# Kernel tuning notes

Hardware: AMD Instinct MI355X
Metric: run time of the kernel (lower is better)

## Reference

```python
import jax, jax.numpy as jnp
import numpy as np

N_NODES = 50000
N_EDGES = 800000
D = 64  # node_dim == edge_dim
NEG_SLOPE = 0.2
EPS = 1e-5


def _lin_params(key, d_in, d_out):
    k1, k2 = jax.random.split(key)
    bound = 1.0 / np.sqrt(d_in)
    W = jax.random.uniform(k1, (d_out, d_in), minval=-bound, maxval=bound, dtype=jnp.float32)
    b = jax.random.uniform(k2, (d_out,), minval=-bound, maxval=bound, dtype=jnp.float32)
    return W, b


def setup_inputs() -> dict:
    key = jax.random.key(0)
    ks = jax.random.split(key, 12)
    V = jax.random.normal(ks[0], (N_NODES, D), dtype=jnp.float32)
    E = jax.random.normal(ks[1], (N_EDGES, D), dtype=jnp.float32)
    src = jax.random.randint(ks[2], (N_EDGES,), 0, N_NODES, dtype=jnp.int32)
    dst = jax.random.randint(ks[3], (N_EDGES,), 0, N_NODES, dtype=jnp.int32)
    pA_w, pA_b = _lin_params(ks[4], D, D)   # NodePooling.A
    pB_w, pB_b = _lin_params(ks[5], D, D)   # NodePooling.B
    mW1, mb1 = _lin_params(ks[6], D, D)     # edge MLP layer 1
    mW2, mb2 = _lin_params(ks[7], D, D)     # edge MLP layer 2
    BW, Bb = _lin_params(ks[8], D, D)       # GenMessage.B (scale)
    CW, Cb = _lin_params(ks[9], D, D)       # GenMessage.C (shift)
    return {"V": V, "E": E, "src": src, "dst": dst,
            "pA_w": pA_w, "pA_b": pA_b, "pB_w": pB_w, "pB_b": pB_b,
            "mW1": mW1, "mb1": mb1, "mW2": mW2, "mb2": mb2,
            "BW": BW, "Bb": Bb, "CW": CW, "Cb": Cb}


def _lrelu(x):
    return jnp.where(x >= 0, x, NEG_SLOPE * x)


def reference(V, E, src, dst, pA_w, pA_b, pB_w, pB_b, mW1, mb1, mW2, mb2, BW, Bb, CW, Cb):
    n = V.shape[0]
    # V = act(V); NodePooling: B(lrelu(A(V)))
    Va = _lrelu(V)
    Vp = _lrelu(Va @ pA_w.T + pA_b) @ pB_w.T + pB_b  # [N, D]
    # edge MLP on edge features (2 Linear+ReLU layers)
    x = jax.nn.relu(E @ mW1.T + mb1)
    x = jax.nn.relu(x @ mW2.T + mb2)                  # [E, D]
    scale = jax.nn.sigmoid(x @ BW.T + Bb)
    shift = x @ CW.T + Cb
    # gathered src features, gated affine message
    M1 = scale * Vp[src] + shift                      # [E, D]
    M2 = M1 * M1
    # segment-mean onto dst (DGL fn.mean); zero for isolated nodes
    deg = jax.ops.segment_sum(jnp.ones((dst.shape[0],), jnp.float32), dst, num_segments=n)
    denom = jnp.maximum(deg, 1.0)[:, None]
    V1 = jax.ops.segment_sum(M1, dst, num_segments=n) / denom
    V2 = jax.ops.segment_sum(M2, dst, num_segments=n) / denom
    return jnp.sqrt(jax.nn.relu(V2 - V1) + EPS)
```

## Files before the change

### kernel.cpp

```cpp
#include <hip/hip_runtime.h>

#define NN 50000
#define NE 800000
#define DDIM 64
#define PADX 68
#define PADS 68
#define NB_SCAN ((NN + 255) / 256)
#define NEG_SLOPE 0.2f
#define EPS_V 1e-5f

typedef short bf16x8 __attribute__((ext_vector_type(8)));
typedef float f32x4 __attribute__((ext_vector_type(4)));

__device__ __forceinline__ float lrelu_f(float x) { return x >= 0.0f ? x : NEG_SLOPE * x; }

__device__ __forceinline__ unsigned short bf16_rn(float x) {
    union { float f; unsigned int u; } c; c.f = x;
    unsigned int r = c.u + 0x7FFF + ((c.u >> 16) & 1);
    return (unsigned short)(r >> 16);
}
__device__ __forceinline__ float bf16_tof(unsigned short h) {
    union { float f; unsigned int u; } c; c.u = ((unsigned int)h) << 16;
    return c.f;
}

__device__ __forceinline__ void split8(const float* __restrict__ v, bf16x8& h, bf16x8& l)
{
    #pragma unroll
    for (int j = 0; j < 8; ++j) {
        unsigned short hh = bf16_rn(v[j]);
        h[j] = (short)hh;
        l[j] = (short)bf16_rn(v[j] - bf16_tof(hh));
    }
}

__device__ __forceinline__ void mma_tile(float acc[16], const float* __restrict__ XT,
                                         const float* __restrict__ Wc, int e0, int f0)
{
    #pragma unroll 4
    for (int kk = 0; kk < DDIM; kk += 4) {
        float4 A0 = *(const float4*)&XT[(kk+0)*PADX + e0];
        float4 A1 = *(const float4*)&XT[(kk+1)*PADX + e0];
        float4 A2 = *(const float4*)&XT[(kk+2)*PADX + e0];
        float4 A3 = *(const float4*)&XT[(kk+3)*PADX + e0];
        float4 B0 = *(const float4*)&Wc[(f0+0)*PADX + kk];
        float4 B1 = *(const float4*)&Wc[(f0+1)*PADX + kk];
        float4 B2 = *(const float4*)&Wc[(f0+2)*PADX + kk];
        float4 B3 = *(const float4*)&Wc[(f0+3)*PADX + kk];
        const float a[4][4] = {{A0.x,A0.y,A0.z,A0.w},{A1.x,A1.y,A1.z,A1.w},
                               {A2.x,A2.y,A2.z,A2.w},{A3.x,A3.y,A3.z,A3.w}};
        const float b[4][4] = {{B0.x,B0.y,B0.z,B0.w},{B1.x,B1.y,B1.z,B1.w},
                               {B2.x,B2.y,B2.z,B2.w},{B3.x,B3.y,B3.z,B3.w}};
        #pragma unroll
        for (int j = 0; j < 4; ++j)
            #pragma unroll
            for (int i = 0; i < 4; ++i)
                #pragma unroll
                for (int q = 0; q < 4; ++q)
                    acc[i*4+j] = fmaf(a[q][i], b[j][q], acc[i*4+j]);
    }
}

__device__ __forceinline__ void load_w_f32(float* __restrict__ Wc, const float* __restrict__ Wg, int tid)
{
    #pragma unroll
    for (int c = 0; c < 4; ++c) {
        int idx = (c << 10) + (tid << 2);
        int f = idx >> 6, k = idx & 63;
        *(float4*)&Wc[f*PADX + k] = *(const float4*)&Wg[idx];
    }
}

__global__ __launch_bounds__(256, 3)
void node_pool_kernel(const float* __restrict__ V,
                      const float* __restrict__ Aw, const float* __restrict__ Ab,
                      const float* __restrict__ Bw, const float* __restrict__ Bbv,
                      float* __restrict__ Vp,
                      const int* __restrict__ dst, int* __restrict__ degi)
{
    __shared__ float Wc[DDIM*PADX];
    __shared__ float XT[DDIM*PADX];
    const int tid = threadIdx.x;
    const int nb = blockIdx.x * 64;
    const int e0 = (tid & 15) << 2;
    const int f0 = (tid >> 4) << 2;

    #pragma unroll
    for (int c = 0; c < 4; ++c) {
        int idx = (c << 10) + (tid << 2);
        int e = idx >> 6, d = idx & 63;
        int row = nb + e; if (row > NN-1) row = NN-1;
        float4 v = *(const float4*)&V[(size_t)row*DDIM + d];
        XT[(d+0)*PADX + e] = lrelu_f(v.x);
        XT[(d+1)*PADX + e] = lrelu_f(v.y);
        XT[(d+2)*PADX + e] = lrelu_f(v.z);
        XT[(d+3)*PADX + e] = lrelu_f(v.w);
    }
    load_w_f32(Wc, Aw, tid);
    __syncthreads();

    float acc[16];
    #pragma unroll
    for (int i = 0; i < 16; ++i) acc[i] = 0.f;
    mma_tile(acc, XT, Wc, e0, f0);
    __syncthreads();

    {
        float4 bv = *(const float4*)&Ab[f0];
        const float ba[4] = {bv.x, bv.y, bv.z, bv.w};
        #pragma unroll
        for (int j = 0; j < 4; ++j) {
            float4 v;
            v.x = lrelu_f(acc[0*4+j] + ba[j]);
            v.y = lrelu_f(acc[1*4+j] + ba[j]);
            v.z = lrelu_f(acc[2*4+j] + ba[j]);
            v.w = lrelu_f(acc[3*4+j] + ba[j]);
            *(float4*)&XT[(f0+j)*PADX + e0] = v;
        }
    }
    load_w_f32(Wc, Bw, tid);
    __syncthreads();

    float acc2[16];
    #pragma unroll
    for (int i = 0; i < 16; ++i) acc2[i] = 0.f;
    mma_tile(acc2, XT, Wc, e0, f0);

    float4 bv = *(const float4*)&Bbv[f0];
    #pragma unroll
    for (int i = 0; i < 4; ++i) {
        int row = nb + e0 + i;
        if (row < NN) {
            float4 o;
            o.x = acc2[i*4+0] + bv.x;
            o.y = acc2[i*4+1] + bv.y;
            o.z = acc2[i*4+2] + bv.z;
            o.w = acc2[i*4+3] + bv.w;
            *(float4*)&Vp[(size_t)row*DDIM + f0] = o;
        }
    }

    const int stride = gridDim.x * 256;
    for (int e = blockIdx.x * 256 + tid; e < NE; e += stride)
        atomicAdd(&degi[dst[e]], 1);
}

__global__ __launch_bounds__(256)
void prep_w_kernel(const float* __restrict__ W1, const float* __restrict__ W2,
                   const float* __restrict__ WB, const float* __restrict__ WC,
                   short* __restrict__ WF)
{
    int gid = blockIdx.x * 256 + threadIdx.x;
    int L = gid >> 12, r = gid & 4095;
    int t = r >> 10, ks = (r >> 9) & 1, lane = (r >> 3) & 63, j = r & 7;
    const float* Ws = (L == 0) ? W1 : (L == 1) ? W2 : (L == 2) ? WB : WC;
    int n = lane & 15, kg = lane >> 4;
    int f = t*16 + n, k = ks*32 + kg*8 + j;
    float v = Ws[f*64 + k];
    unsigned short h = bf16_rn(v);
    unsigned short l = bf16_rn(v - bf16_tof(h));
    int base = L*8192 + ((t*2 + ks)*2)*512 + lane*8 + j;
    WF[base]       = (short)h;
    WF[base + 512] = (short)l;
}

__global__ __launch_bounds__(256)
void scan1_kernel(const int* __restrict__ degi, int* __restrict__ linc, int* __restrict__ bsum)
{
    __shared__ int ws[4];
    const int tid = threadIdx.x;
    const int lane = tid & 63, wv = tid >> 6;
    int i = blockIdx.x * 256 + tid;
    int v = (i < NN) ? degi[i] : 0;
    int sc = v;
    #pragma unroll
    for (int off = 1; off < 64; off <<= 1) {
        int t = __shfl_up(sc, off, 64);
        if (lane >= off) sc += t;
    }
    if (lane == 63) ws[wv] = sc;
    __syncthreads();
    int wb = 0;
    #pragma unroll
    for (int w = 0; w < 4; ++w) if (w < wv) wb += ws[w];
    int incl = sc + wb;
    if (i < NN) linc[i] = incl;
    if (tid == 255) bsum[blockIdx.x] = incl;
}

__global__ __launch_bounds__(256)
void scan23_kernel(const int* __restrict__ degi, const int* __restrict__ linc,
                   const int* __restrict__ bsum, int* __restrict__ curs)
{
    __shared__ int ws[4];
    __shared__ int base_s;
    const int tid = threadIdx.x;
    const int lane = tid & 63, wv = tid >> 6;
    int v = (tid < NB_SCAN) ? bsum[tid] : 0;
    int sc = v;
    #pragma unroll
    for (int off = 1; off < 64; off <<= 1) {
        int t = __shfl_up(sc, off, 64);
        if (lane >= off) sc += t;
    }
    if (lane == 63) ws[wv] = sc;
    __syncthreads();
    int wb = 0;
    #pragma unroll
    for (int w = 0; w < 4; ++w) if (w < wv) wb += ws[w];
    if (tid == blockIdx.x) base_s = sc + wb - v;
    __syncthreads();
    int i = blockIdx.x * 256 + tid;
    if (i < NN) curs[i] = base_s + linc[i] - degi[i];
}

__global__ __launch_bounds__(256)
void scatter_kernel(const int* __restrict__ dst, int* __restrict__ cursor, int* __restrict__ eidx)
{
    int e = blockIdx.x * 256 + threadIdx.x;
    if (e < NE) {
        int p = atomicAdd(&cursor[dst[e]], 1);
        eidx[p] = e;
    }
}

__device__ __forceinline__ void gemm64_dual(const short* __restrict__ WL, int lane,
                                            const bf16x8 ah0[2], const bf16x8 al0[2],
                                            const bf16x8 ah1[2], const bf16x8 al1[2],
                                            f32x4 acc0[4], f32x4 acc1[4])
{
    #pragma unroll
    for (int ks = 0; ks < 2; ++ks) {
        bf16x8 bh[4], bl[4];
        #pragma unroll
        for (int t = 0; t < 4; ++t) {
            bh[t] = *(const bf16x8*)&WL[(((t*2 + ks)*2 + 0)*64 + lane)*8];
            bl[t] = *(const bf16x8*)&WL[(((t*2 + ks)*2 + 1)*64 + lane)*8];
        }
        #pragma unroll
        for (int t = 0; t < 4; ++t) {
            acc0[t] = __builtin_amdgcn_mfma_f32_16x16x32_bf16(al0[ks], bh[t], acc0[t], 0, 0, 0);
            acc1[t] = __builtin_amdgcn_mfma_f32_16x16x32_bf16(al1[ks], bh[t], acc1[t], 0, 0, 0);
            acc0[t] = __builtin_amdgcn_mfma_f32_16x16x32_bf16(ah0[ks], bl[t], acc0[t], 0, 0, 0);
            acc1[t] = __builtin_amdgcn_mfma_f32_16x16x32_bf16(ah1[ks], bl[t], acc1[t], 0, 0, 0);
            acc0[t] = __builtin_amdgcn_mfma_f32_16x16x32_bf16(ah0[ks], bh[t], acc0[t], 0, 0, 0);
            acc1[t] = __builtin_amdgcn_mfma_f32_16x16x32_bf16(ah1[ks], bh[t], acc1[t], 0, 0, 0);
        }
    }
}

__device__ __forceinline__ void transpose_frags_dual(float* __restrict__ sw,
                                                     const f32x4 y0[4], const f32x4 y1[4],
                                                     int lane,
                                                     bf16x8 ah0[2], bf16x8 al0[2],
                                                     bf16x8 ah1[2], bf16x8 al1[2])
{
    const int n = lane & 15, mg = lane >> 4;
    #pragma unroll
    for (int t = 0; t < 4; ++t)
        #pragma unroll
        for (int r = 0; r < 4; ++r) {
            sw[(mg*4 + r)*PADS + t*16 + n]      = y0[t][r];
            sw[(16 + mg*4 + r)*PADS + t*16 + n] = y1[t][r];
        }
    __builtin_amdgcn_wave_barrier();
    const int m = lane & 15, kg = lane >> 4;
    {
        float x[16];
        *(float4*)&x[0]  = *(const float4*)&sw[m*PADS + kg*8];
        *(float4*)&x[4]  = *(const float4*)&sw[m*PADS + kg*8 + 4];
        *(float4*)&x[8]  = *(const float4*)&sw[m*PADS + 32 + kg*8];
        *(float4*)&x[12] = *(const float4*)&sw[m*PADS + 32 + kg*8 + 4];
        split8(&x[0], ah0[0], al0[0]);
        split8(&x[8], ah0[1], al0[1]);
    }
    {
        float x[16];
        *(float4*)&x[0]  = *(const float4*)&sw[(16+m)*PADS + kg*8];
        *(float4*)&x[4]  = *(const float4*)&sw[(16+m)*PADS + kg*8 + 4];
        *(float4*)&x[8]  = *(const float4*)&sw[(16+m)*PADS + 32 + kg*8];
        *(float4*)&x[12] = *(const float4*)&sw[(16+m)*PADS + 32 + kg*8 + 4];
        split8(&x[0], ah1[0], al1[0]);
        split8(&x[8], ah1[1], al1[1]);
    }
    __builtin_amdgcn_wave_barrier();
}

__global__ __launch_bounds__(256, 3)
void edge_kernel(const float* __restrict__ Eg,
                 const int* __restrict__ src, const int* __restrict__ dst,
                 const int* __restrict__ eidx,
                 const short* __restrict__ WF,
                 const float* __restrict__ b1, const float* __restrict__ b2,
                 const float* __restrict__ bB, const float* __restrict__ bC,
                 const float* __restrict__ Vp,
                 float* __restrict__ S1, float* __restrict__ S2)
{
    __shared__ float scratch[4 * 32 * PADS];
    __shared__ int aux[4 * 64];

    const int tid = threadIdx.x;
    const int lane = tid & 63, wv = tid >> 6;
    float* sw = scratch + wv * 32 * PADS;
    int* auxw = aux + wv * 64;

    const int ew = blockIdx.x * 128 + wv * 32;
    const int m = lane & 15, kg = lane >> 4;

    if (lane < 32) {
        int eg = eidx[ew + lane];
        auxw[lane]      = src[eg];
        auxw[32 + lane] = dst[eg];
    }
    bf16x8 ah0[2], al0[2], ah1[2], al1[2];
    {
        int eg0 = eidx[ew + m];
        int eg1 = eidx[ew + 16 + m];
        const float* er0 = Eg + (size_t)eg0*DDIM + kg*8;
        const float* er1 = Eg + (size_t)eg1*DDIM + kg*8;
        float x[16];
        *(float4*)&x[0]  = *(const float4*)&er0[0];
        *(float4*)&x[4]  = *(const float4*)&er0[4];
        *(float4*)&x[8]  = *(const float4*)&er0[32];
        *(float4*)&x[12] = *(const float4*)&er0[36];
        split8(&x[0], ah0[0], al0[0]);
        split8(&x[8], ah0[1], al0[1]);
        *(float4*)&x[0]  = *(const float4*)&er1[0];
        *(float4*)&x[4]  = *(const float4*)&er1[4];
        *(float4*)&x[8]  = *(const float4*)&er1[32];
        *(float4*)&x[12] = *(const float4*)&er1[36];
        split8(&x[0], ah1[0], al1[0]);
        split8(&x[8], ah1[1], al1[1]);
    }

    const int n = lane & 15, mg = lane >> 4;

    f32x4 acc0[4], acc1[4];
    #pragma unroll
    for (int t = 0; t < 4; ++t) { acc0[t] = (f32x4){0.f,0.f,0.f,0.f}; acc1[t] = (f32x4){0.f,0.f,0.f,0.f}; }
    gemm64_dual(WF, lane, ah0, al0, ah1, al1, acc0, acc1);
    #pragma unroll
    for (int t = 0; t < 4; ++t) {
        float b = b1[t*16 + n];
        #pragma unroll
        for (int r = 0; r < 4; ++r) {
            acc0[t][r] = fmaxf(acc0[t][r] + b, 0.0f);
            acc1[t][r] = fmaxf(acc1[t][r] + b, 0.0f);
        }
    }
    transpose_frags_dual(sw, acc0, acc1, lane, ah0, al0, ah1, al1);

    #pragma unroll
    for (int t = 0; t < 4; ++t) { acc0[t] = (f32x4){0.f,0.f,0.f,0.f}; acc1[t] = (f32x4){0.f,0.f,0.f,0.f}; }
    gemm64_dual(WF + 8192, lane, ah0, al0, ah1, al1, acc0, acc1);
    #pragma unroll
    for (int t = 0; t < 4; ++t) {
        float b = b2[t*16 + n];
        #pragma unroll
        for (int r = 0; r < 4; ++r) {
            acc0[t][r] = fmaxf(acc0[t][r] + b, 0.0f);
            acc1[t][r] = fmaxf(acc1[t][r] + b, 0.0f);
        }
    }
    transpose_frags_dual(sw, acc0, acc1, lane, ah0, al0, ah1, al1);

    f32x4 accS0[4], accS1[4], accH0[4], accH1[4];
    #pragma unroll
    for (int t = 0; t < 4; ++t) {
        accS0[t] = (f32x4){0.f,0.f,0.f,0.f}; accS1[t] = (f32x4){0.f,0.f,0.f,0.f};
        accH0[t] = (f32x4){0.f,0.f,0.f,0.f}; accH1[t] = (f32x4){0.f,0.f,0.f,0.f};
    }
    gemm64_dual(WF + 2*8192, lane, ah0, al0, ah1, al1, accS0, accS1);
    gemm64_dual(WF + 3*8192, lane, ah0, al0, ah1, al1, accH0, accH1);

    {
        int sn0[4], sn1[4];
        #pragma unroll
        for (int r = 0; r < 4; ++r) { sn0[r] = auxw[mg*4 + r]; sn1[r] = auxw[16 + mg*4 + r]; }
        #pragma unroll
        for (int t = 0; t < 4; ++t) {
            const int f = t*16 + n;
            const float bBv = bB[f];
            const float bCv = bC[f];
            #pragma unroll
            for (int r = 0; r < 4; ++r) {
                float vp0 = Vp[(size_t)sn0[r]*DDIM + f];
                float sg0 = 1.0f / (1.0f + __expf(-(accS0[t][r] + bBv)));
                sw[(mg*4 + r)*PADS + f] = fmaf(sg0, vp0, accH0[t][r] + bCv);
                float vp1 = Vp[(size_t)sn1[r]*DDIM + f];
                float sg1 = 1.0f / (1.0f + __expf(-(accS1[t][r] + bBv)));
                sw[(16 + mg*4 + r)*PADS + f] = fmaf(sg1, vp1, accH1[t][r] + bCv);
            }
        }
    }
    __builtin_amdgcn_wave_barrier();

    const int f = lane;
    float s1 = 0.f, s2 = 0.f;
    int prev = auxw[32];
    #pragma unroll 4
    for (int e = 0; e < 32; ++e) {
        int dn = auxw[32 + e];
        float m1 = sw[e*PADS + f];
        float m2 = m1 * m1;
        if (dn != prev) {
            atomicAdd(&S1[(size_t)prev*DDIM + f], s1);
            atomicAdd(&S2[(size_t)prev*DDIM + f], s2);
            s1 = 0.f; s2 = 0.f; prev = dn;
        }
        s1 += m1; s2 += m2;
    }
    atomicAdd(&S1[(size_t)prev*DDIM + f], s1);
    atomicAdd(&S2[(size_t)prev*DDIM + f], s2);
}

__global__ __launch_bounds__(256)
void finalize_kernel(const float* __restrict__ S1, const float* __restrict__ S2,
                     const int* __restrict__ degi, float* __restrict__ out)
{
    int gid = blockIdx.x * blockDim.x + threadIdx.x;
    if (gid >= NN*DDIM) return;
    int n = gid >> 6;
    float dn = (float)degi[n];
    dn = dn > 1.0f ? dn : 1.0f;
    float v = (S2[gid] - S1[gid]) / dn;
    out[gid] = sqrtf(fmaxf(v, 0.0f) + EPS_V);
}

extern "C" void kernel_launch(void* const* d_in, const int* in_sizes, int n_in,
                              void* d_out, int out_size, void* d_ws, size_t ws_size,
                              hipStream_t stream) {
    const float* V   = (const float*)d_in[0];
    const float* Eg  = (const float*)d_in[1];
    const int*   src = (const int*)d_in[2];
    const int*   dst = (const int*)d_in[3];
    const float* pAw = (const float*)d_in[4];
    const float* pAb = (const float*)d_in[5];
    const float* pBw = (const float*)d_in[6];
    const float* pBb = (const float*)d_in[7];
    const float* mW1 = (const float*)d_in[8];
    const float* mb1 = (const float*)d_in[9];
    const float* mW2 = (const float*)d_in[10];
    const float* mb2 = (const float*)d_in[11];
    const float* BW  = (const float*)d_in[12];
    const float* Bb  = (const float*)d_in[13];
    const float* CW  = (const float*)d_in[14];
    const float* Cb  = (const float*)d_in[15];
    float* out = (float*)d_out;

    float* ws    = (float*)d_ws;
    float* Vp    = ws;
    float* S1    = ws + (size_t)NN*DDIM;
    float* S2    = ws + (size_t)2*NN*DDIM;
    int*   degi  = (int*)(ws + (size_t)3*NN*DDIM);
    int*   curs  = degi + NN;
    int*   linc  = curs + NN;
    int*   bsum  = linc + NN;
    int*   bbase = bsum + NB_SCAN;
    int*   eidx  = bbase + NB_SCAN;
    short* WF    = (short*)(eidx + NE);

    hipMemsetAsync(S1, 0, (size_t)(2*NN*DDIM + NN) * sizeof(float), stream);

    prep_w_kernel<<<64, 256, 0, stream>>>(mW1, mW2, BW, CW, WF);
    node_pool_kernel<<<(NN + 63)/64, 256, 0, stream>>>(V, pAw, pAb, pBw, pBb, Vp, dst, degi);
    scan1_kernel<<<NB_SCAN, 256, 0, stream>>>(degi, linc, bsum);
    scan23_kernel<<<NB_SCAN, 256, 0, stream>>>(degi, linc, bsum, curs);
    scatter_kernel<<<(NE + 255)/256, 256, 0, stream>>>(dst, curs, eidx);
    edge_kernel<<<NE/128, 256, 0, stream>>>(Eg, src, dst, eidx, WF,
                                            mb1, mb2, Bb, Cb, Vp, S1, S2);
    finalize_kernel<<<(NN*DDIM + 255)/256, 256, 0, stream>>>(S1, S2, degi, out);
}
```

Measured before the change: 577.7 us.

## Make edge kernel persistent over contiguous sorted groups with plain stores for interior segments

The edge kernel now launches a fixed 4096 waves, and each wave walks a contiguous range of 32-edge groups in dst-sorted order. Running segment sums carry across groups, so a node segment that lies wholly inside one wave's range is written with plain stores. Only the first and last segments of each range still use atomics. The bf16 hi/lo split also switches to the packed v_cvt_pk_bf16_f32 instruction. The trade-off is less parallelism and latency hiding per launch, since each wave now runs its groups serially.

Result: slower. 788.1 us (+36.4%).

```diff
diff --git a/kernel.cpp b/kernel.cpp
--- a/kernel.cpp
+++ b/kernel.cpp
@@ -9,6 +9,11 @@
 #define NEG_SLOPE 0.2f
 #define EPS_V 1e-5f
 
+#define NGROUPS (NE / 32)
+#define NWAVES_E 4096
+#define GQ (NGROUPS / NWAVES_E)
+#define GR (NGROUPS - NWAVES_E * GQ)
+
 typedef short bf16x8 __attribute__((ext_vector_type(8)));
 typedef float f32x4 __attribute__((ext_vector_type(4)));
 
@@ -24,14 +29,27 @@
     return c.f;
 }
 
+__device__ __forceinline__ unsigned cvtpk_bf16(float a, float b) {
+    unsigned r;
+    asm("v_cvt_pk_bf16_f32 %0, %1, %2" : "=v"(r) : "v"(a), "v"(b));
+    return r;
+}
+
 __device__ __forceinline__ void split8(const float* __restrict__ v, bf16x8& h, bf16x8& l)
 {
-    #pragma unroll
-    for (int j = 0; j < 8; ++j) {
-        unsigned short hh = bf16_rn(v[j]);
-        h[j] = (short)hh;
-        l[j] = (short)bf16_rn(v[j] - bf16_tof(hh));
-    }
+    union { bf16x8 v8; unsigned u[4]; } H, L;
+    #pragma unroll
+    for (int k = 0; k < 4; ++k) {
+        float a = v[2*k], b = v[2*k+1];
+        unsigned p = cvtpk_bf16(a, b);
+        union { float f; unsigned u; } h0, h1;
+        h0.u = p << 16;
+        h1.u = p & 0xFFFF0000u;
+        unsigned q = cvtpk_bf16(a - h0.f, b - h1.f);
+        H.u[k] = p;
+        L.u[k] = q;
+    }
+    h = H.v8; l = L.v8;
 }
 
 __device__ __forceinline__ void mma_tile(float acc[16], const float* __restrict__ XT,
@@ -304,114 +322,134 @@
     float* sw = scratch + wv * 32 * PADS;
     int* auxw = aux + wv * 64;
 
-    const int ew = blockIdx.x * 128 + wv * 32;
+    const int gw = blockIdx.x * 4 + wv;
+    int g0, gn;
+    if (gw < GR) { g0 = gw * (GQ + 1); gn = GQ + 1; }
+    else         { g0 = GR * (GQ + 1) + (gw - GR) * GQ; gn = GQ; }
+
     const int m = lane & 15, kg = lane >> 4;
-
-    if (lane < 32) {
-        int eg = eidx[ew + lane];
-        auxw[lane]      = src[eg];
-        auxw[32 + lane] = dst[eg];
-    }
-    bf16x8 ah0[2], al0[2], ah1[2], al1[2];
-    {
-        int eg0 = eidx[ew + m];
-        int eg1 = eidx[ew + 16 + m];
-        const float* er0 = Eg + (size_t)eg0*DDIM + kg*8;
-        const float* er1 = Eg + (size_t)eg1*DDIM + kg*8;
-        float x[16];
-        *(float4*)&x[0]  = *(const float4*)&er0[0];
-        *(float4*)&x[4]  = *(const float4*)&er0[4];
-        *(float4*)&x[8]  = *(const float4*)&er0[32];
-        *(float4*)&x[12] = *(const float4*)&er0[36];
-        split8(&x[0], ah0[0], al0[0]);
-        split8(&x[8], ah0[1], al0[1]);
-        *(float4*)&x[0]  = *(const float4*)&er1[0];
-        *(float4*)&x[4]  = *(const float4*)&er1[4];
-        *(float4*)&x[8]  = *(const float4*)&er1[32];
-        *(float4*)&x[12] = *(const float4*)&er1[36];
-        split8(&x[0], ah1[0], al1[0]);
-        split8(&x[8], ah1[1], al1[1]);
-    }
-
     const int n = lane & 15, mg = lane >> 4;
-
-    f32x4 acc0[4], acc1[4];
-    #pragma unroll
-    for (int t = 0; t < 4; ++t) { acc0[t] = (f32x4){0.f,0.f,0.f,0.f}; acc1[t] = (f32x4){0.f,0.f,0.f,0.f}; }
-    gemm64_dual(WF, lane, ah0, al0, ah1, al1, acc0, acc1);
-    #pragma unroll
-    for (int t = 0; t < 4; ++t) {
-        float b = b1[t*16 + n];
-        #pragma unroll
-        for (int r = 0; r < 4; ++r) {
-            acc0[t][r] = fmaxf(acc0[t][r] + b, 0.0f);
-            acc1[t][r] = fmaxf(acc1[t][r] + b, 0.0f);
-        }
-    }
-    transpose_frags_dual(sw, acc0, acc1, lane, ah0, al0, ah1, al1);
-
-    #pragma unroll
-    for (int t = 0; t < 4; ++t) { acc0[t] = (f32x4){0.f,0.f,0.f,0.f}; acc1[t] = (f32x4){0.f,0.f,0.f,0.f}; }
-    gemm64_dual(WF + 8192, lane, ah0, al0, ah1, al1, acc0, acc1);
-    #pragma unroll
-    for (int t = 0; t < 4; ++t) {
-        float b = b2[t*16 + n];
-        #pragma unroll
-        for (int r = 0; r < 4; ++r) {
-            acc0[t][r] = fmaxf(acc0[t][r] + b, 0.0f);
-            acc1[t][r] = fmaxf(acc1[t][r] + b, 0.0f);
-        }
-    }
-    transpose_frags_dual(sw, acc0, acc1, lane, ah0, al0, ah1, al1);
-
-    f32x4 accS0[4], accS1[4], accH0[4], accH1[4];
-    #pragma unroll
-    for (int t = 0; t < 4; ++t) {
-        accS0[t] = (f32x4){0.f,0.f,0.f,0.f}; accS1[t] = (f32x4){0.f,0.f,0.f,0.f};
-        accH0[t] = (f32x4){0.f,0.f,0.f,0.f}; accH1[t] = (f32x4){0.f,0.f,0.f,0.f};
-    }
-    gemm64_dual(WF + 2*8192, lane, ah0, al0, ah1, al1, accS0, accS1);
-    gemm64_dual(WF + 3*8192, lane, ah0, al0, ah1, al1, accH0, accH1);
-
-    {
-        int sn0[4], sn1[4];
-        #pragma unroll
-        for (int r = 0; r < 4; ++r) { sn0[r] = auxw[mg*4 + r]; sn1[r] = auxw[16 + mg*4 + r]; }
+    const int f = lane;
+
+    float s1 = 0.f, s2 = 0.f;
+    int prev = -1;
+    int seg_atomic = 1;
+
+    for (int g = 0; g < gn; ++g) {
+        const int ew = (g0 + g) * 32;
+
+        if (lane < 32) {
+            int eg = eidx[ew + lane];
+            auxw[lane]      = src[eg];
+            auxw[32 + lane] = dst[eg];
+        }
+        bf16x8 ah0[2], al0[2], ah1[2], al1[2];
+        {
+            int eg0 = eidx[ew + m];
+            int eg1 = eidx[ew + 16 + m];
+            const float* er0 = Eg + (size_t)eg0*DDIM + kg*8;
+            const float* er1 = Eg + (size_t)eg1*DDIM + kg*8;
+            float x[16];
+            *(float4*)&x[0]  = *(const float4*)&er0[0];
+            *(float4*)&x[4]  = *(const float4*)&er0[4];
+            *(float4*)&x[8]  = *(const float4*)&er0[32];
+            *(float4*)&x[12] = *(const float4*)&er0[36];
+            split8(&x[0], ah0[0], al0[0]);
+            split8(&x[8], ah0[1], al0[1]);
+            *(float4*)&x[0]  = *(const float4*)&er1[0];
+            *(float4*)&x[4]  = *(const float4*)&er1[4];
+            *(float4*)&x[8]  = *(const float4*)&er1[32];
+            *(float4*)&x[12] = *(const float4*)&er1[36];
+            split8(&x[0], ah1[0], al1[0]);
+            split8(&x[8], ah1[1], al1[1]);
+        }
+
+        f32x4 acc0[4], acc1[4];
+        #pragma unroll
+        for (int t = 0; t < 4; ++t) { acc0[t] = (f32x4){0.f,0.f,0.f,0.f}; acc1[t] = (f32x4){0.f,0.f,0.f,0.f}; }
+        gemm64_dual(WF, lane, ah0, al0, ah1, al1, acc0, acc1);
         #pragma unroll
         for (int t = 0; t < 4; ++t) {
-            const int f = t*16 + n;
-            const float bBv = bB[f];
-            const float bCv = bC[f];
+            float b = b1[t*16 + n];
             #pragma unroll
             for (int r = 0; r < 4; ++r) {
-                float vp0 = Vp[(size_t)sn0[r]*DDIM + f];
-                float sg0 = 1.0f / (1.0f + __expf(-(accS0[t][r] + bBv)));
-                sw[(mg*4 + r)*PADS + f] = fmaf(sg0, vp0, accH0[t][r] + bCv);
-                float vp1 = Vp[(size_t)sn1[r]*DDIM + f];
-                float sg1 = 1.0f / (1.0f + __expf(-(accS1[t][r] + bBv)));
-                sw[(16 + mg*4 + r)*PADS + f] = fmaf(sg1, vp1, accH1[t][r] + bCv);
+                acc0[t][r] = fmaxf(acc0[t][r] + b, 0.0f);
+                acc1[t][r] = fmaxf(acc1[t][r] + b, 0.0f);
             }
         }
-    }
-    __builtin_amdgcn_wave_barrier();
-
-    const int f = lane;
-    float s1 = 0.f, s2 = 0.f;
-    int prev = auxw[32];
-    #pragma unroll 4
-    for (int e = 0; e < 32; ++e) {
-        int dn = auxw[32 + e];
-        float m1 = sw[e*PADS + f];
-        float m2 = m1 * m1;
-        if (dn != prev) {
-            atomicAdd(&S1[(size_t)prev*DDIM + f], s1);
-            atomicAdd(&S2[(size_t)prev*DDIM + f], s2);
-            s1 = 0.f; s2 = 0.f; prev = dn;
-        }
-        s1 += m1; s2 += m2;
-    }
-    atomicAdd(&S1[(size_t)prev*DDIM + f], s1);
-    atomicAdd(&S2[(size_t)prev*DDIM + f], s2);
+        transpose_frags_dual(sw, acc0, acc1, lane, ah0, al0, ah1, al1);
+
+        #pragma unroll
+        for (int t = 0; t < 4; ++t) { acc0[t] = (f32x4){0.f,0.f,0.f,0.f}; acc1[t] = (f32x4){0.f,0.f,0.f,0.f}; }
+        gemm64_dual(WF + 8192, lane, ah0, al0, ah1, al1, acc0, acc1);
+        #pragma unroll
+        for (int t = 0; t < 4; ++t) {
+            float b = b2[t*16 + n];
+            #pragma unroll
+            for (int r = 0; r < 4; ++r) {
+                acc0[t][r] = fmaxf(acc0[t][r] + b, 0.0f);
+                acc1[t][r] = fmaxf(acc1[t][r] + b, 0.0f);
+            }
+        }
+        transpose_frags_dual(sw, acc0, acc1, lane, ah0, al0, ah1, al1);
+
+        f32x4 accS0[4], accS1[4], accH0[4], accH1[4];
+        #pragma unroll
+        for (int t = 0; t < 4; ++t) {
+            accS0[t] = (f32x4){0.f,0.f,0.f,0.f}; accS1[t] = (f32x4){0.f,0.f,0.f,0.f};
+            accH0[t] = (f32x4){0.f,0.f,0.f,0.f}; accH1[t] = (f32x4){0.f,0.f,0.f,0.f};
+        }
+        gemm64_dual(WF + 2*8192, lane, ah0, al0, ah1, al1, accS0, accS1);
+        gemm64_dual(WF + 3*8192, lane, ah0, al0, ah1, al1, accH0, accH1);
+
+        {
+            int sn0[4], sn1[4];
+            #pragma unroll
+            for (int r = 0; r < 4; ++r) { sn0[r] = auxw[mg*4 + r]; sn1[r] = auxw[16 + mg*4 + r]; }
+            #pragma unroll
+            for (int t = 0; t < 4; ++t) {
+                const int ff = t*16 + n;
+                const float bBv = bB[ff];
+                const float bCv = bC[ff];
+                #pragma unroll
+                for (int r = 0; r < 4; ++r) {
+                    float vp0 = Vp[(size_t)sn0[r]*DDIM + ff];
+                    float sg0 = 1.0f / (1.0f + __expf(-(accS0[t][r] + bBv)));
+                    sw[(mg*4 + r)*PADS + ff] = fmaf(sg0, vp0, accH0[t][r] + bCv);
+                    float vp1 = Vp[(size_t)sn1[r]*DDIM + ff];
+                    float sg1 = 1.0f / (1.0f + __expf(-(accS1[t][r] + bBv)));
+                    sw[(16 + mg*4 + r)*PADS + ff] = fmaf(sg1, vp1, accH1[t][r] + bCv);
+                }
+            }
+        }
+        __builtin_amdgcn_wave_barrier();
+
+        #pragma unroll 4
+        for (int e = 0; e < 32; ++e) {
+            int dn = auxw[32 + e];
+            float m1 = sw[e*PADS + f];
+            float m2 = m1 * m1;
+            if (dn != prev) {
+                if (prev >= 0) {
+                    if (seg_atomic) {
+                        atomicAdd(&S1[(size_t)prev*DDIM + f], s1);
+                        atomicAdd(&S2[(size_t)prev*DDIM + f], s2);
+                    } else {
+                        S1[(size_t)prev*DDIM + f] = s1;
+                        S2[(size_t)prev*DDIM + f] = s2;
+                    }
+                    seg_atomic = 0;
+                }
+                s1 = 0.f; s2 = 0.f; prev = dn;
+            }
+            s1 += m1; s2 += m2;
+        }
+        __builtin_amdgcn_wave_barrier();
+    }
+    if (prev >= 0) {
+        atomicAdd(&S1[(size_t)prev*DDIM + f], s1);
+        atomicAdd(&S2[(size_t)prev*DDIM + f], s2);
+    }
 }
 
 __global__ __launch_bounds__(256)
@@ -467,7 +505,7 @@
     scan1_kernel<<<NB_SCAN, 256, 0, stream>>>(degi, linc, bsum);
     scan23_kernel<<<NB_SCAN, 256, 0, stream>>>(degi, linc, bsum, curs);
     scatter_kernel<<<(NE + 255)/256, 256, 0, stream>>>(dst, curs, eidx);
-    edge_kernel<<<NE/128, 256, 0, stream>>>(Eg, src, dst, eidx, WF,
-                                            mb1, mb2, Bb, Cb, Vp, S1, S2);
+    edge_kernel<<<NWAVES_E/4, 256, 0, stream>>>(Eg, src, dst, eidx, WF,
+                                                mb1, mb2, Bb, Cb, Vp, S1, S2);
     finalize_kernel<<<(NN*DDIM + 255)/256, 256, 0, stream>>>(S1, S2, degi, out);
 }
```
